# Kernel tuning notes

Hardware: AMD Instinct MI355X
Metric: run time of the kernel (lower is better)

## Reference

```python
import jax, jax.numpy as jnp
import numpy as np


def setup_inputs() -> dict:
    key = jax.random.key(0)
    ks = jax.random.split(key, 5)
    B, S, H, I, E = 4, 2048, 1024, 4096, 8
    scale_in = 1.0 / np.sqrt(H)
    scale_mid = 1.0 / np.sqrt(I)
    return {
        "x": jax.random.normal(ks[0], (B, S, H), dtype=jnp.float32),
        "w_gate": jax.random.normal(ks[1], (H, E), dtype=jnp.float32) * scale_in,
        "w1": jax.random.normal(ks[2], (E, H, I), dtype=jnp.float32) * scale_in,
        "w2": jax.random.normal(ks[3], (E, I, H), dtype=jnp.float32) * scale_mid,
        "w3": jax.random.normal(ks[4], (E, H, I), dtype=jnp.float32) * scale_in,
        "num_experts_per_tok": 2,
    }


def reference(x, w_gate, w1, w2, w3, num_experts_per_tok):
    """MoE with top-k routing and SwiGLU experts (Mixtral-style).

    x: [B, S, H]; w_gate: [H, E]; w1/w3: [E, H, I]; w2: [E, I, H].
    Returns [B, S, H]. Matches torch module output (aux_loss is a side
    attribute in the original, not returned).
    """
    B, S, H = x.shape
    E = w_gate.shape[1]
    K = num_experts_per_tok
    xf = x.reshape(-1, H)                           # [T, H]

    logits = xf @ w_gate                            # [T, E]
    probs = jax.nn.softmax(logits, axis=-1)
    topk_probs, topk_idx = jax.lax.top_k(probs, K)  # [T, K]
    topk_probs = topk_probs / topk_probs.sum(axis=-1, keepdims=True)

    # Per-token per-expert combine weight: sum over k of renormalized top-k
    # probs mapped back to expert slots. [T, E]
    comb = jnp.sum(jax.nn.one_hot(topk_idx, E, dtype=xf.dtype)
                   * topk_probs[..., None], axis=1)

    out = jnp.zeros_like(xf)
    for e in range(E):  # small fixed loop over experts
        hidden = jax.nn.silu(xf @ w1[e]) * (xf @ w3[e])  # [T, I]
        out = out + (hidden @ w2[e]) * comb[:, e:e + 1]
    return out.reshape(B, S, H)
```

## Files before the change

kernel.cpp:

```cpp
#include <hip/hip_runtime.h>

typedef unsigned short u16;
typedef __attribute__((ext_vector_type(4))) float f32x4;
typedef __attribute__((ext_vector_type(8))) short s16x8;

#define T_TOK 8192
#define HD    1024
#define ID    4096
#define NE    8
#define AK    (T_TOK * 2)
#define APAD  (AK + 256)
#define MTMAX 72

#define BAR()   __builtin_amdgcn_s_barrier()
#define SB0()   __builtin_amdgcn_sched_barrier(0)
#define PRIO1() __builtin_amdgcn_s_setprio(1)
#define PRIO0() __builtin_amdgcn_s_setprio(0)
#define WAITV6() asm volatile("s_waitcnt vmcnt(6)" ::: "memory")
#define WAITV8() asm volatile("s_waitcnt vmcnt(8)" ::: "memory")
#define LGKM0()  do { asm volatile("s_waitcnt lgkmcnt(0)" ::: "memory"); SB0(); } while (0)

__device__ __forceinline__ u16 f2bf(float f) {
  unsigned u = __builtin_bit_cast(unsigned, f);
  u += 0x7FFFu + ((u >> 16) & 1u);
  return (u16)(u >> 16);
}

__device__ __forceinline__ void gld16(u16* lds, const u16* g) {
  __builtin_amdgcn_global_load_lds(
      (const __attribute__((address_space(1))) unsigned int*)g,
      (__attribute__((address_space(3))) unsigned int*)lds, 16, 0, 0);
}


__global__ void k_init(int* counts) {
  if (threadIdx.x < NE) counts[threadIdx.x] = 0;
}

__global__ __launch_bounds__(256) void k_router(
    const float* __restrict__ x, const float* __restrict__ wg,
    int* __restrict__ tidx, float* __restrict__ tw, int* __restrict__ counts) {
  __shared__ float wgs[NE * HD];
  int tid = threadIdx.x;
  for (int i = tid; i < NE * HD; i += 256) {
    int h = i >> 3, e = i & 7;
    wgs[e * HD + h] = wg[i];
  }
  __syncthreads();
  int lane = tid & 63, wid = tid >> 6;
  int t = blockIdx.x * 4 + wid;
  const float* xr = x + (size_t)t * HD;
  double acc[NE];
#pragma unroll
  for (int e = 0; e < NE; ++e) acc[e] = 0.0;
  for (int i = 0; i < HD / 64; ++i) {
    float xv = xr[lane + i * 64];
#pragma unroll
    for (int e = 0; e < NE; ++e)
      acc[e] += (double)xv * (double)wgs[e * HD + lane + i * 64];
  }
#pragma unroll
  for (int e = 0; e < NE; ++e)
    for (int s = 32; s >= 1; s >>= 1) acc[e] += __shfl_xor(acc[e], s, 64);
  int e0 = 0; double m0 = acc[0];
  for (int e = 1; e < NE; ++e) if (acc[e] > m0) { m0 = acc[e]; e0 = e; }
  int e1 = -1; double m1 = -1e300;
  for (int e = 0; e < NE; ++e) if (e != e0 && acc[e] > m1) { m1 = acc[e]; e1 = e; }
  if (lane == 0) {
    double d = exp(m1 - m0);
    tidx[t * 2] = e0; tidx[t * 2 + 1] = e1;
    tw[t * 2] = (float)(1.0 / (1.0 + d));
    tw[t * 2 + 1] = (float)(d / (1.0 + d));
    atomicAdd(&counts[e0], 1);
    atomicAdd(&counts[e1], 1);
  }
}

__global__ void k_offsets(const int* __restrict__ counts, int* offs, int* cursors,
                          int* __restrict__ tiles, int* __restrict__ ntile) {
  if (threadIdx.x == 0) {
    int s = 0;
    for (int e = 0; e < NE; ++e) { offs[e] = s; s += counts[e]; }
    offs[NE] = s;
    int nt = 0;
    for (int e = 0; e < NE; ++e)
      for (int m0 = 0; m0 < counts[e]; m0 += 256)
        tiles[nt++] = (e << 16) | (m0 >> 8);
    ntile[0] = nt;
    for (int i = nt; i < MTMAX; ++i) tiles[i] = 0;
  }
  if (threadIdx.x < NE) cursors[threadIdx.x] = 0;
}

__global__ __launch_bounds__(256) void k_scatter(
    const int* __restrict__ tidx, const int* __restrict__ offs,
    int* cursors, const float* __restrict__ tw,
    int* __restrict__ list, float* __restrict__ wlist) {
  int idx = blockIdx.x * 256 + threadIdx.x;
  if (idx >= AK) return;
  int e = tidx[idx];
  int p = atomicAdd(&cursors[e], 1);
  int a = offs[e] + p;
  list[a] = idx >> 1;
  wlist[a] = tw[idx];
}


__global__ __launch_bounds__(256) void k_cvtx(const float* __restrict__ in,
                                              u16* __restrict__ out) {
  int idx = blockIdx.x * 256 + threadIdx.x;
  const float4* in4 = (const float4*)in;
  float4 v = in4[idx];
  ushort4 o;
  o.x = f2bf(v.x); o.y = f2bf(v.y); o.z = f2bf(v.z); o.w = f2bf(v.w);
  ((ushort4*)out)[idx] = o;
}

__global__ __launch_bounds__(256) void k_tconv(const float* __restrict__ in,
                                               u16* __restrict__ out, int R, int C) {
  __shared__ u16 tile[64][72];
  size_t base = (size_t)blockIdx.z * R * C;
  int r0 = blockIdx.y * 64, c0 = blockIdx.x * 64;
  int t = threadIdx.x;
  int rr = t >> 4, cc = (t & 15) * 4;
#pragma unroll
  for (int i = 0; i < 4; ++i) {
    int r = i * 16 + rr;
    float4 v = *(const float4*)&in[base + (size_t)(r0 + r) * C + c0 + cc];
    tile[cc + 0][r] = f2bf(v.x);
    tile[cc + 1][r] = f2bf(v.y);
    tile[cc + 2][r] = f2bf(v.z);
    tile[cc + 3][r] = f2bf(v.w);
  }
  __syncthreads();
  int c = t >> 3, ch = (t & 7) * 8;
#pragma unroll
  for (int j = 0; j < 2; ++j) {
    int cr = j * 32 + c;
    *(s16x8*)&out[base + (size_t)(c0 + cr) * R + r0 + ch] =
        *(const s16x8*)&tile[cr][ch];
  }
}

__global__ __launch_bounds__(256) void k_tconv13(const float* __restrict__ w1,
                                                 const float* __restrict__ w3,
                                                 u16* __restrict__ out) {
  __shared__ u16 tile[64][72];
  int which = blockIdx.z >> 3, e = blockIdx.z & 7;
  const float* in = (which ? w3 : w1) + (size_t)e * HD * ID;
  int r0 = blockIdx.y * 64, c0 = blockIdx.x * 64;
  int t = threadIdx.x;
  int rr = t >> 4, cc = (t & 15) * 4;
#pragma unroll
  for (int i = 0; i < 4; ++i) {
    int r = i * 16 + rr;
    float4 v = *(const float4*)&in[(size_t)(r0 + r) * ID + c0 + cc];
    tile[cc + 0][r] = f2bf(v.x);
    tile[cc + 1][r] = f2bf(v.y);
    tile[cc + 2][r] = f2bf(v.z);
    tile[cc + 3][r] = f2bf(v.w);
  }
  __syncthreads();
  int c = t >> 3, ch = (t & 7) * 8;
#pragma unroll
  for (int j = 0; j < 2; ++j) {
    int crow = c0 + j * 32 + c;
    int pr = ((crow >> 4) << 5) + which * 16 + (crow & 15);
    *(s16x8*)&out[((size_t)e * 2 * ID + pr) * HD + r0 + ch] =
        *(const s16x8*)&tile[j * 32 + c][ch];
  }
}


#define GEMM_CORE(NTK, NITER) \
  int wr = wid >> 2, wc = wid & 3; \
  int lane15 = lane & 15, lq = lane >> 4, sw8 = lane15 & 7; \
  f32x4 acc[8][4]; \
  _Pragma("unroll") for (int m = 0; m < 8; ++m) \
    _Pragma("unroll") for (int n = 0; n < 4; ++n) acc[m][n] = (f32x4){0.f,0.f,0.f,0.f}; \
  auto stgA = [&](int bb, int h, int kt) { \
    gld16(&As[bb][(h*128 + 0*64 + wid*8) * 64], gA[h*2+0] + kt*64); \
    gld16(&As[bb][(h*128 + 1*64 + wid*8) * 64], gA[h*2+1] + kt*64); }; \
  auto stgB = [&](int bb, int h, int kt) { \
    gld16(&Bs[bb][(h*128 + 0*64 + wid*8) * 64], gB[h*2+0] + kt*64); \
    gld16(&Bs[bb][(h*128 + 1*64 + wid*8) * 64], gB[h*2+1] + kt*64); }; \
  s16x8 a[4][2], b[2][2]; \
  auto rdA = [&](int bb, int mh) { \
    _Pragma("unroll") for (int mm = 0; mm < 4; ++mm) \
      _Pragma("unroll") for (int kk = 0; kk < 2; ++kk) \
        a[mm][kk] = *(const s16x8*)&As[bb][(mh*128 + wr*64 + mm*16 + lane15)*64 + (((kk*4+lq)^sw8)*8)]; }; \
  auto rdB = [&](int bb, int fh) { \
    _Pragma("unroll") for (int ff = 0; ff < 2; ++ff) \
      _Pragma("unroll") for (int kk = 0; kk < 2; ++kk) \
        b[ff][kk] = *(const s16x8*)&Bs[bb][(fh*128 + wc*32 + ff*16 + lane15)*64 + (((kk*4+lq)^sw8)*8)]; }; \
  auto mf = [&](int mh, int fh) { \
    _Pragma("unroll") for (int mm = 0; mm < 4; ++mm) \
      _Pragma("unroll") for (int ff = 0; ff < 2; ++ff) { \
        acc[mh*4+mm][fh*2+ff] = __builtin_amdgcn_mfma_f32_16x16x32_bf16(a[mm][0], b[ff][0], acc[mh*4+mm][fh*2+ff], 0, 0, 0); \
        acc[mh*4+mm][fh*2+ff] = __builtin_amdgcn_mfma_f32_16x16x32_bf16(a[mm][1], b[ff][1], acc[mh*4+mm][fh*2+ff], 0, 0, 0); } }; \
   \
  stgA(0,0,0); stgB(0,0,0); stgA(0,1,0); stgB(0,1,0); stgA(1,0,1); stgB(1,0,1); \
  WAITV8(); BAR(); SB0(); \
  for (int i = 0; i < (NITER); ++i) { \
    int ku2 = (2*i+2) & ((NTK)-1), ku3 = (2*i+3) & ((NTK)-1); \
     rdA(0,0); rdB(0,0); stgA(1,1,2*i+1); WAITV6(); BAR(); LGKM0(); PRIO1(); mf(0,0); PRIO0(); BAR(); SB0(); \
     rdB(0,1); stgB(1,1,2*i+1); BAR(); LGKM0(); PRIO1(); mf(0,1); PRIO0(); BAR(); SB0(); \
     rdA(0,1); rdB(0,0); stgA(0,0,ku2); BAR(); LGKM0(); PRIO1(); mf(1,0); PRIO0(); BAR(); SB0(); \
     rdB(0,1); stgB(0,0,ku2); WAITV8(); BAR(); LGKM0(); PRIO1(); mf(1,1); PRIO0(); BAR(); SB0(); \
     rdA(1,0); rdB(1,0); stgA(0,1,ku2); WAITV6(); BAR(); LGKM0(); PRIO1(); mf(0,0); PRIO0(); BAR(); SB0(); \
     rdB(1,1); stgB(0,1,ku2); BAR(); LGKM0(); PRIO1(); mf(0,1); PRIO0(); BAR(); SB0(); \
     rdA(1,1); rdB(1,0); stgA(1,0,ku3); BAR(); LGKM0(); PRIO1(); mf(1,0); PRIO0(); BAR(); SB0(); \
     rdB(1,1); stgB(1,0,ku3); WAITV8(); BAR(); LGKM0(); PRIO1(); mf(1,1); PRIO0(); BAR(); SB0(); \
  }

__global__ __launch_bounds__(512, 1) void k_gemm1(
    const u16* __restrict__ xb, const u16* __restrict__ w13b,
    const int* __restrict__ list, const int* __restrict__ offs,
    const int* __restrict__ tiles, const int* __restrict__ ntile,
    u16* __restrict__ hidden) {
  int ti = blockIdx.y;
  if (ti >= ntile[0]) return;
  int packed = tiles[ti];
  int e = packed >> 16;
  int m0 = (packed & 0xFFFF) << 8;
  int aoff = offs[e];
  int cnt = offs[e + 1] - aoff;
  int n0 = blockIdx.x * 256;

  __shared__ u16 As[2][256 * 64];
  __shared__ u16 Bs[2][256 * 64];

  int tid = threadIdx.x, lane = tid & 63, wid = tid >> 6;
  int l8 = lane >> 3, c8 = lane & 7;
  int csrc = (c8 ^ l8) * 8;

  const u16* gA[4]; const u16* gB[4];
#pragma unroll
  for (int h = 0; h < 2; ++h)
#pragma unroll
    for (int c = 0; c < 2; ++c) {
      int row = h * 128 + c * 64 + wid * 8 + l8;
      int rr = m0 + row; if (rr > cnt - 1) rr = cnt - 1;
      gA[h*2+c] = xb + (size_t)list[aoff + rr] * HD + csrc;
      gB[h*2+c] = w13b + ((size_t)e * 2 * ID + n0 + row) * HD + csrc;
    }

  GEMM_CORE(HD / 64, HD / 128)

#pragma unroll
  for (int mh = 0; mh < 2; ++mh)
#pragma unroll
    for (int mm = 0; mm < 4; ++mm)
#pragma unroll
      for (int j = 0; j < 4; ++j) {
        int grow = m0 + mh * 128 + wr * 64 + mm * 16 + lq * 4 + j;
        if (grow < cnt) {
          size_t rbase = (size_t)(aoff + grow) * ID;
#pragma unroll
          for (int p = 0; p < 2; ++p) {
            float v1 = acc[mh*4+mm][2*p][j];
            float v3 = acc[mh*4+mm][2*p+1][j];
            float s = v1 / (1.0f + __expf(-v1));
            int icol = ((n0 + p * 128 + wc * 32) >> 1) + lane15;
            hidden[rbase + icol] = f2bf(s * v3);
          }
        }
      }
}

__global__ __launch_bounds__(512, 1) void k_gemm2(
    const u16* __restrict__ hidden, const u16* __restrict__ w2b,
    const int* __restrict__ offs, const int* __restrict__ list,
    const float* __restrict__ wlist, const int* __restrict__ tiles,
    const int* __restrict__ ntile, float* __restrict__ out) {
  int ti = blockIdx.y;
  if (ti >= ntile[0]) return;
  int packed = tiles[ti];
  int e = packed >> 16;
  int m0 = (packed & 0xFFFF) << 8;
  int aoff = offs[e];
  int cnt = offs[e + 1] - aoff;
  int n0 = (blockIdx.x & 3) * 256;
  int kc = (blockIdx.x >> 2) * 2048;

  __shared__ u16 As[2][256 * 64];
  __shared__ u16 Bs[2][256 * 64];

  int tid = threadIdx.x, lane = tid & 63, wid = tid >> 6;
  int l8 = lane >> 3, c8 = lane & 7;
  int csrc = (c8 ^ l8) * 8;

  const u16* gA[4]; const u16* gB[4];
#pragma unroll
  for (int h = 0; h < 2; ++h)
#pragma unroll
    for (int c = 0; c < 2; ++c) {
      int row = h * 128 + c * 64 + wid * 8 + l8;
      gA[h*2+c] = hidden + (size_t)(aoff + m0 + row) * ID + kc + csrc;
      gB[h*2+c] = w2b + ((size_t)e * HD + n0 + row) * ID + kc + csrc;
    }

  GEMM_CORE(2048 / 64, 2048 / 128)

#pragma unroll
  for (int mh = 0; mh < 2; ++mh)
#pragma unroll
    for (int mm = 0; mm < 4; ++mm)
#pragma unroll
      for (int j = 0; j < 4; ++j) {
        int grow = m0 + mh * 128 + wr * 64 + mm * 16 + lq * 4 + j;
        if (grow < cnt) {
          int a_ = aoff + grow;
          int tok = list[a_];
          float wgt = wlist[a_];
          float* orow = out + (size_t)tok * HD;
#pragma unroll
          for (int f = 0; f < 4; ++f) {
            int col = n0 + (f >> 1) * 128 + wc * 32 + (f & 1) * 16 + lane15;
            atomicAdd(&orow[col], wgt * acc[mh*4+mm][f][j]);
          }
        }
      }
}


extern "C" void kernel_launch(void* const* d_in, const int* in_sizes, int n_in,
                              void* d_out, int out_size, void* d_ws, size_t ws_size,
                              hipStream_t stream) {
  const float* x  = (const float*)d_in[0];
  const float* wg = (const float*)d_in[1];
  const float* w1 = (const float*)d_in[2];
  const float* w2 = (const float*)d_in[3];
  const float* w3 = (const float*)d_in[4];

  char* p = (char*)d_ws;
  auto alloc = [&](size_t bytes) {
    char* r = p;
    p += (bytes + 255) & ~(size_t)255;
    return r;
  };
  u16*   xb      = (u16*)alloc((size_t)T_TOK * HD * 2);
  u16*   w13b    = (u16*)alloc((size_t)NE * 2 * ID * HD * 2);
  u16*   w2b     = (u16*)alloc((size_t)NE * HD * ID * 2);
  u16*   hidden  = (u16*)alloc((size_t)APAD * ID * 2);
  int*   tidx    = (int*)alloc(AK * 4);
  float* tw      = (float*)alloc(AK * 4);
  int*   list    = (int*)alloc(AK * 4);
  float* wlist   = (float*)alloc(AK * 4);
  int*   counts  = (int*)alloc(64);
  int*   offs    = (int*)alloc(64);
  int*   cursors = (int*)alloc(64);
  int*   tiles   = (int*)alloc(MTMAX * 4);
  int*   ntile   = (int*)alloc(64);
  (void)ws_size; (void)in_sizes; (void)n_in;

  hipMemsetAsync(d_out, 0, (size_t)out_size * 4, stream);

  k_init<<<1, 64, 0, stream>>>(counts);
  k_router<<<T_TOK / 4, 256, 0, stream>>>(x, wg, tidx, tw, counts);
  k_offsets<<<1, 64, 0, stream>>>(counts, offs, cursors, tiles, ntile);
  k_scatter<<<AK / 256, 256, 0, stream>>>(tidx, offs, cursors, tw, list, wlist);

  k_cvtx<<<(T_TOK * HD / 4) / 256, 256, 0, stream>>>(x, xb);
  dim3 g13(ID / 64, HD / 64, 2 * NE);
  k_tconv13<<<g13, 256, 0, stream>>>(w1, w3, w13b);
  dim3 g2(HD / 64, ID / 64, NE);
  k_tconv<<<g2, 256, 0, stream>>>(w2, w2b, ID, HD);

  dim3 gg1(2 * ID / 256, MTMAX, 1);
  k_gemm1<<<gg1, 512, 0, stream>>>(xb, w13b, list, offs, tiles, ntile, hidden);
  dim3 gg2(8, MTMAX, 1);
  k_gemm2<<<gg2, 512, 0, stream>>>(hidden, w2b, offs, list, wlist, tiles, ntile,
                                   (float*)d_out);
}
```

Before: 1.035 ms.

## Fuse prep kernels into one launch, cache B fragments, split gemm2 K further

Merges the router, x conversion and both weight transpose-convert kernels into a single block-indexed prep kernel, which removes launch gaps and lets the phases overlap. The GEMM core now keeps B fragments for both column halves in registers, so the second pair of MFMA phases no longer re-reads B from LDS. This raises register pressure. gemm2 splits K into four 1024-wide chunks instead of two, doubling its grid for better occupancy at the cost of more atomic adds into the output.

```diff
diff --git a/kernel.cpp b/kernel.cpp
--- a/kernel.cpp
+++ b/kernel.cpp
@@ -35,45 +35,6 @@
 
 __global__ void k_init(int* counts) {
   if (threadIdx.x < NE) counts[threadIdx.x] = 0;
-}
-
-__global__ __launch_bounds__(256) void k_router(
-    const float* __restrict__ x, const float* __restrict__ wg,
-    int* __restrict__ tidx, float* __restrict__ tw, int* __restrict__ counts) {
-  __shared__ float wgs[NE * HD];
-  int tid = threadIdx.x;
-  for (int i = tid; i < NE * HD; i += 256) {
-    int h = i >> 3, e = i & 7;
-    wgs[e * HD + h] = wg[i];
-  }
-  __syncthreads();
-  int lane = tid & 63, wid = tid >> 6;
-  int t = blockIdx.x * 4 + wid;
-  const float* xr = x + (size_t)t * HD;
-  double acc[NE];
-#pragma unroll
-  for (int e = 0; e < NE; ++e) acc[e] = 0.0;
-  for (int i = 0; i < HD / 64; ++i) {
-    float xv = xr[lane + i * 64];
-#pragma unroll
-    for (int e = 0; e < NE; ++e)
-      acc[e] += (double)xv * (double)wgs[e * HD + lane + i * 64];
-  }
-#pragma unroll
-  for (int e = 0; e < NE; ++e)
-    for (int s = 32; s >= 1; s >>= 1) acc[e] += __shfl_xor(acc[e], s, 64);
-  int e0 = 0; double m0 = acc[0];
-  for (int e = 1; e < NE; ++e) if (acc[e] > m0) { m0 = acc[e]; e0 = e; }
-  int e1 = -1; double m1 = -1e300;
-  for (int e = 0; e < NE; ++e) if (e != e0 && acc[e] > m1) { m1 = acc[e]; e1 = e; }
-  if (lane == 0) {
-    double d = exp(m1 - m0);
-    tidx[t * 2] = e0; tidx[t * 2 + 1] = e1;
-    tw[t * 2] = (float)(1.0 / (1.0 + d));
-    tw[t * 2 + 1] = (float)(d / (1.0 + d));
-    atomicAdd(&counts[e0], 1);
-    atomicAdd(&counts[e1], 1);
-  }
 }
 
 __global__ void k_offsets(const int* __restrict__ counts, int* offs, int* cursors,
@@ -106,68 +67,118 @@
 }
 
 
-__global__ __launch_bounds__(256) void k_cvtx(const float* __restrict__ in,
-                                              u16* __restrict__ out) {
-  int idx = blockIdx.x * 256 + threadIdx.x;
-  const float4* in4 = (const float4*)in;
-  float4 v = in4[idx];
-  ushort4 o;
-  o.x = f2bf(v.x); o.y = f2bf(v.y); o.z = f2bf(v.z); o.w = f2bf(v.w);
-  ((ushort4*)out)[idx] = o;
-}
-
-__global__ __launch_bounds__(256) void k_tconv(const float* __restrict__ in,
-                                               u16* __restrict__ out, int R, int C) {
-  __shared__ u16 tile[64][72];
-  size_t base = (size_t)blockIdx.z * R * C;
-  int r0 = blockIdx.y * 64, c0 = blockIdx.x * 64;
-  int t = threadIdx.x;
-  int rr = t >> 4, cc = (t & 15) * 4;
-#pragma unroll
-  for (int i = 0; i < 4; ++i) {
-    int r = i * 16 + rr;
-    float4 v = *(const float4*)&in[base + (size_t)(r0 + r) * C + c0 + cc];
-    tile[cc + 0][r] = f2bf(v.x);
-    tile[cc + 1][r] = f2bf(v.y);
-    tile[cc + 2][r] = f2bf(v.z);
-    tile[cc + 3][r] = f2bf(v.w);
-  }
-  __syncthreads();
-  int c = t >> 3, ch = (t & 7) * 8;
-#pragma unroll
-  for (int j = 0; j < 2; ++j) {
-    int cr = j * 32 + c;
-    *(s16x8*)&out[base + (size_t)(c0 + cr) * R + r0 + ch] =
-        *(const s16x8*)&tile[cr][ch];
-  }
-}
-
-__global__ __launch_bounds__(256) void k_tconv13(const float* __restrict__ w1,
-                                                 const float* __restrict__ w3,
-                                                 u16* __restrict__ out) {
-  __shared__ u16 tile[64][72];
-  int which = blockIdx.z >> 3, e = blockIdx.z & 7;
-  const float* in = (which ? w3 : w1) + (size_t)e * HD * ID;
-  int r0 = blockIdx.y * 64, c0 = blockIdx.x * 64;
-  int t = threadIdx.x;
-  int rr = t >> 4, cc = (t & 15) * 4;
-#pragma unroll
-  for (int i = 0; i < 4; ++i) {
-    int r = i * 16 + rr;
-    float4 v = *(const float4*)&in[(size_t)(r0 + r) * ID + c0 + cc];
-    tile[cc + 0][r] = f2bf(v.x);
-    tile[cc + 1][r] = f2bf(v.y);
-    tile[cc + 2][r] = f2bf(v.z);
-    tile[cc + 3][r] = f2bf(v.w);
-  }
-  __syncthreads();
-  int c = t >> 3, ch = (t & 7) * 8;
-#pragma unroll
-  for (int j = 0; j < 2; ++j) {
-    int crow = c0 + j * 32 + c;
-    int pr = ((crow >> 4) << 5) + which * 16 + (crow & 15);
-    *(s16x8*)&out[((size_t)e * 2 * ID + pr) * HD + r0 + ch] =
-        *(const s16x8*)&tile[j * 32 + c][ch];
+#define NB_CVT 8192
+#define NB_T13 16384
+#define NB_T2  8192
+#define NB_RTR 2048
+
+__global__ __launch_bounds__(256) void k_prep(
+    const float* __restrict__ x, const float* __restrict__ wg,
+    const float* __restrict__ w1, const float* __restrict__ w2,
+    const float* __restrict__ w3,
+    u16* __restrict__ xb, u16* __restrict__ w13b, u16* __restrict__ w2b,
+    int* __restrict__ tidx, float* __restrict__ tw, int* __restrict__ counts) {
+  __shared__ char smem[32768];
+  int bid = blockIdx.x, t = threadIdx.x;
+
+  if (bid < NB_CVT) {
+    int idx = bid * 256 + t;
+    float4 v = ((const float4*)x)[idx];
+    ushort4 o;
+    o.x = f2bf(v.x); o.y = f2bf(v.y); o.z = f2bf(v.z); o.w = f2bf(v.w);
+    ((ushort4*)xb)[idx] = o;
+    return;
+  }
+  if (bid < NB_CVT + NB_T13) {
+    u16 (*tile)[72] = (u16(*)[72])smem;
+    int r = bid - NB_CVT;
+    int bx = r & 63, by = (r >> 6) & 15, bz = r >> 10;
+    int which = bz >> 3, e = bz & 7;
+    const float* in = (which ? w3 : w1) + (size_t)e * HD * ID;
+    int r0 = by * 64, c0 = bx * 64;
+    int rr = t >> 4, cc = (t & 15) * 4;
+#pragma unroll
+    for (int i = 0; i < 4; ++i) {
+      int rw = i * 16 + rr;
+      float4 v = *(const float4*)&in[(size_t)(r0 + rw) * ID + c0 + cc];
+      tile[cc + 0][rw] = f2bf(v.x);
+      tile[cc + 1][rw] = f2bf(v.y);
+      tile[cc + 2][rw] = f2bf(v.z);
+      tile[cc + 3][rw] = f2bf(v.w);
+    }
+    __syncthreads();
+    int c = t >> 3, ch = (t & 7) * 8;
+#pragma unroll
+    for (int j = 0; j < 2; ++j) {
+      int crow = c0 + j * 32 + c;
+      int pr = ((crow >> 4) << 5) + which * 16 + (crow & 15);
+      *(s16x8*)&w13b[((size_t)e * 2 * ID + pr) * HD + r0 + ch] =
+          *(const s16x8*)&tile[j * 32 + c][ch];
+    }
+    return;
+  }
+  if (bid < NB_CVT + NB_T13 + NB_T2) {
+    u16 (*tile)[72] = (u16(*)[72])smem;
+    int r = bid - NB_CVT - NB_T13;
+    int bx = r & 15, by = (r >> 4) & 63, bz = r >> 10;
+    const int R = ID, C = HD;
+    size_t base = (size_t)bz * R * C;
+    int r0 = by * 64, c0 = bx * 64;
+    int rr = t >> 4, cc = (t & 15) * 4;
+#pragma unroll
+    for (int i = 0; i < 4; ++i) {
+      int rw = i * 16 + rr;
+      float4 v = *(const float4*)&w2[base + (size_t)(r0 + rw) * C + c0 + cc];
+      tile[cc + 0][rw] = f2bf(v.x);
+      tile[cc + 1][rw] = f2bf(v.y);
+      tile[cc + 2][rw] = f2bf(v.z);
+      tile[cc + 3][rw] = f2bf(v.w);
+    }
+    __syncthreads();
+    int c = t >> 3, ch = (t & 7) * 8;
+#pragma unroll
+    for (int j = 0; j < 2; ++j) {
+      int cr = j * 32 + c;
+      *(s16x8*)&w2b[base + (size_t)(c0 + cr) * R + r0 + ch] =
+          *(const s16x8*)&tile[cr][ch];
+    }
+    return;
+  }
+  {
+    float* wgs = (float*)smem;
+    int blockR = bid - NB_CVT - NB_T13 - NB_T2;
+    for (int i = t; i < NE * HD; i += 256) {
+      int h = i >> 3, e = i & 7;
+      wgs[e * HD + h] = wg[i];
+    }
+    __syncthreads();
+    int lane = t & 63, wid = t >> 6;
+    int tok = blockR * 4 + wid;
+    const float* xr = x + (size_t)tok * HD;
+    double acc[NE];
+#pragma unroll
+    for (int e = 0; e < NE; ++e) acc[e] = 0.0;
+    for (int i = 0; i < HD / 64; ++i) {
+      float xv = xr[lane + i * 64];
+#pragma unroll
+      for (int e = 0; e < NE; ++e)
+        acc[e] += (double)xv * (double)wgs[e * HD + lane + i * 64];
+    }
+#pragma unroll
+    for (int e = 0; e < NE; ++e)
+      for (int s = 32; s >= 1; s >>= 1) acc[e] += __shfl_xor(acc[e], s, 64);
+    int e0 = 0; double m0 = acc[0];
+    for (int e = 1; e < NE; ++e) if (acc[e] > m0) { m0 = acc[e]; e0 = e; }
+    int e1 = -1; double m1 = -1e300;
+    for (int e = 0; e < NE; ++e) if (e != e0 && acc[e] > m1) { m1 = acc[e]; e1 = e; }
+    if (lane == 0) {
+      double d = exp(m1 - m0);
+      tidx[tok * 2] = e0; tidx[tok * 2 + 1] = e1;
+      tw[tok * 2] = (float)(1.0 / (1.0 + d));
+      tw[tok * 2 + 1] = (float)(d / (1.0 + d));
+      atomicAdd(&counts[e0], 1);
+      atomicAdd(&counts[e1], 1);
+    }
   }
 }
 
@@ -184,7 +195,7 @@
   auto stgB = [&](int bb, int h, int kt) { \
     gld16(&Bs[bb][(h*128 + 0*64 + wid*8) * 64], gB[h*2+0] + kt*64); \
     gld16(&Bs[bb][(h*128 + 1*64 + wid*8) * 64], gB[h*2+1] + kt*64); }; \
-  s16x8 a[4][2], b[2][2]; \
+  s16x8 a[4][2], b[4][2]; \
   auto rdA = [&](int bb, int mh) { \
     _Pragma("unroll") for (int mm = 0; mm < 4; ++mm) \
       _Pragma("unroll") for (int kk = 0; kk < 2; ++kk) \
@@ -192,12 +203,12 @@
   auto rdB = [&](int bb, int fh) { \
     _Pragma("unroll") for (int ff = 0; ff < 2; ++ff) \
       _Pragma("unroll") for (int kk = 0; kk < 2; ++kk) \
-        b[ff][kk] = *(const s16x8*)&Bs[bb][(fh*128 + wc*32 + ff*16 + lane15)*64 + (((kk*4+lq)^sw8)*8)]; }; \
+        b[fh*2+ff][kk] = *(const s16x8*)&Bs[bb][(fh*128 + wc*32 + ff*16 + lane15)*64 + (((kk*4+lq)^sw8)*8)]; }; \
   auto mf = [&](int mh, int fh) { \
     _Pragma("unroll") for (int mm = 0; mm < 4; ++mm) \
       _Pragma("unroll") for (int ff = 0; ff < 2; ++ff) { \
-        acc[mh*4+mm][fh*2+ff] = __builtin_amdgcn_mfma_f32_16x16x32_bf16(a[mm][0], b[ff][0], acc[mh*4+mm][fh*2+ff], 0, 0, 0); \
-        acc[mh*4+mm][fh*2+ff] = __builtin_amdgcn_mfma_f32_16x16x32_bf16(a[mm][1], b[ff][1], acc[mh*4+mm][fh*2+ff], 0, 0, 0); } }; \
+        acc[mh*4+mm][fh*2+ff] = __builtin_amdgcn_mfma_f32_16x16x32_bf16(a[mm][0], b[fh*2+ff][0], acc[mh*4+mm][fh*2+ff], 0, 0, 0); \
+        acc[mh*4+mm][fh*2+ff] = __builtin_amdgcn_mfma_f32_16x16x32_bf16(a[mm][1], b[fh*2+ff][1], acc[mh*4+mm][fh*2+ff], 0, 0, 0); } }; \
    \
   stgA(0,0,0); stgB(0,0,0); stgA(0,1,0); stgB(0,1,0); stgA(1,0,1); stgB(1,0,1); \
   WAITV8(); BAR(); SB0(); \
@@ -205,12 +216,12 @@
     int ku2 = (2*i+2) & ((NTK)-1), ku3 = (2*i+3) & ((NTK)-1); \
      rdA(0,0); rdB(0,0); stgA(1,1,2*i+1); WAITV6(); BAR(); LGKM0(); PRIO1(); mf(0,0); PRIO0(); BAR(); SB0(); \
      rdB(0,1); stgB(1,1,2*i+1); BAR(); LGKM0(); PRIO1(); mf(0,1); PRIO0(); BAR(); SB0(); \
-     rdA(0,1); rdB(0,0); stgA(0,0,ku2); BAR(); LGKM0(); PRIO1(); mf(1,0); PRIO0(); BAR(); SB0(); \
-     rdB(0,1); stgB(0,0,ku2); WAITV8(); BAR(); LGKM0(); PRIO1(); mf(1,1); PRIO0(); BAR(); SB0(); \
+     rdA(0,1); stgA(0,0,ku2); BAR(); LGKM0(); PRIO1(); mf(1,0); PRIO0(); BAR(); SB0(); \
+     stgB(0,0,ku2); WAITV8(); BAR(); PRIO1(); mf(1,1); PRIO0(); BAR(); SB0(); \
      rdA(1,0); rdB(1,0); stgA(0,1,ku2); WAITV6(); BAR(); LGKM0(); PRIO1(); mf(0,0); PRIO0(); BAR(); SB0(); \
      rdB(1,1); stgB(0,1,ku2); BAR(); LGKM0(); PRIO1(); mf(0,1); PRIO0(); BAR(); SB0(); \
-     rdA(1,1); rdB(1,0); stgA(1,0,ku3); BAR(); LGKM0(); PRIO1(); mf(1,0); PRIO0(); BAR(); SB0(); \
-     rdB(1,1); stgB(1,0,ku3); WAITV8(); BAR(); LGKM0(); PRIO1(); mf(1,1); PRIO0(); BAR(); SB0(); \
+     rdA(1,1); stgA(1,0,ku3); BAR(); LGKM0(); PRIO1(); mf(1,0); PRIO0(); BAR(); SB0(); \
+     stgB(1,0,ku3); WAITV8(); BAR(); PRIO1(); mf(1,1); PRIO0(); BAR(); SB0(); \
   }
 
 __global__ __launch_bounds__(512, 1) void k_gemm1(
@@ -281,7 +292,7 @@
   int aoff = offs[e];
   int cnt = offs[e + 1] - aoff;
   int n0 = (blockIdx.x & 3) * 256;
-  int kc = (blockIdx.x >> 2) * 2048;
+  int kc = (blockIdx.x >> 2) * 1024;
 
   __shared__ u16 As[2][256 * 64];
   __shared__ u16 Bs[2][256 * 64];
@@ -300,7 +311,7 @@
       gB[h*2+c] = w2b + ((size_t)e * HD + n0 + row) * ID + kc + csrc;
     }
 
-  GEMM_CORE(2048 / 64, 2048 / 128)
+  GEMM_CORE(1024 / 64, 1024 / 128)
 
 #pragma unroll
   for (int mh = 0; mh < 2; ++mh)
@@ -357,19 +368,14 @@
   hipMemsetAsync(d_out, 0, (size_t)out_size * 4, stream);
 
   k_init<<<1, 64, 0, stream>>>(counts);
-  k_router<<<T_TOK / 4, 256, 0, stream>>>(x, wg, tidx, tw, counts);
+  k_prep<<<NB_CVT + NB_T13 + NB_T2 + NB_RTR, 256, 0, stream>>>(
+      x, wg, w1, w2, w3, xb, w13b, w2b, tidx, tw, counts);
   k_offsets<<<1, 64, 0, stream>>>(counts, offs, cursors, tiles, ntile);
   k_scatter<<<AK / 256, 256, 0, stream>>>(tidx, offs, cursors, tw, list, wlist);
 
-  k_cvtx<<<(T_TOK * HD / 4) / 256, 256, 0, stream>>>(x, xb);
-  dim3 g13(ID / 64, HD / 64, 2 * NE);
-  k_tconv13<<<g13, 256, 0, stream>>>(w1, w3, w13b);
-  dim3 g2(HD / 64, ID / 64, NE);
-  k_tconv<<<g2, 256, 0, stream>>>(w2, w2b, ID, HD);
-
   dim3 gg1(2 * ID / 256, MTMAX, 1);
   k_gemm1<<<gg1, 512, 0, stream>>>(xb, w13b, list, offs, tiles, ntile, hidden);
-  dim3 gg2(8, MTMAX, 1);
+  dim3 gg2(16, MTMAX, 1);
   k_gemm2<<<gg2, 512, 0, stream>>>(hidden, w2b, offs, list, wlist, tiles, ntile,
                                    (float*)d_out);
 }
```

New measurement: 1.012 ms. -2.3%, faster.
